# Optimization experiments

Measured on AMD Instinct MI355X. Metric: run time of the kernel, lower is better.

Reference implementation:

```python
import jax, jax.numpy as jnp
import numpy as np

N_NODES = 100000
N_EDGES = 1600000
FEAT, HID, OUT = 256, 128, 64
N_BATCH = 10000
EPS = 1e-5


def gcn_conv(x, src, dst, W, b, n):
    # PyG GCNConv: linear -> add self loops -> sym-normalized scatter-add -> bias
    h = x @ W  # [N, C]
    loop = jnp.arange(n, dtype=src.dtype)
    s = jnp.concatenate([src, loop])
    d = jnp.concatenate([dst, loop])
    deg = jax.ops.segment_sum(jnp.ones_like(d, dtype=h.dtype), d, num_segments=n)
    dinv = jnp.where(deg > 0, jax.lax.rsqrt(deg), 0.0)
    norm = dinv[s] * dinv[d]                    # [E+N]
    msg = h[s] * norm[:, None]                  # gather + scale
    out = jax.ops.segment_sum(msg, d, num_segments=n)  # scatter-add
    return out + b


def batch_norm(x, gamma, beta):
    # training-mode BatchNorm1d: batch statistics, biased variance
    mu = jnp.mean(x, axis=0)
    var = jnp.var(x, axis=0)
    return (x - mu) * jax.lax.rsqrt(var + EPS) * gamma + beta


def setup_inputs() -> dict:
    key = jax.random.key(0)
    ks = jax.random.split(key, 8)
    features = jax.random.normal(ks[0], (N_NODES, FEAT), dtype=jnp.float32)
    edge_index = jax.random.randint(ks[1], (2, N_EDGES), 0, N_NODES, dtype=jnp.int64 if jax.config.jax_enable_x64 else jnp.int32)
    batch_nodes = jax.random.randint(ks[2], (N_BATCH,), 0, N_NODES, dtype=jnp.int32)
    W1 = jax.random.normal(ks[3], (FEAT, HID), dtype=jnp.float32) * (1.0 / np.sqrt(FEAT))
    b1 = jnp.zeros((HID,), jnp.float32)
    gamma1 = jnp.ones((HID,), jnp.float32)
    beta1 = jnp.zeros((HID,), jnp.float32)
    W2 = jax.random.normal(ks[4], (HID, OUT), dtype=jnp.float32) * (1.0 / np.sqrt(HID))
    b2 = jnp.zeros((OUT,), jnp.float32)
    gamma2 = jnp.ones((OUT,), jnp.float32)
    beta2 = jnp.zeros((OUT,), jnp.float32)
    return {"features": features, "edge_index": edge_index, "batch_nodes": batch_nodes,
            "W1": W1, "b1": b1, "gamma1": gamma1, "beta1": beta1,
            "W2": W2, "b2": b2, "gamma2": gamma2, "beta2": beta2}


def reference(features, edge_index, batch_nodes, W1, b1, gamma1, beta1, W2, b2, gamma2, beta2):
    src, dst = edge_index[0], edge_index[1]
    n = features.shape[0]
    x = gcn_conv(features, src, dst, W1, b1, n)
    x = jax.nn.relu(batch_norm(x, gamma1, beta1))
    # dropout treated as identity (deterministic reference)
    x = gcn_conv(x, src, dst, W2, b2, n)
    x = jax.nn.relu(batch_norm(x, gamma2, beta2))
    return jax.nn.log_softmax(x[batch_nodes], axis=1)
```

## Files before the change

### kernel.cpp

```cpp
#include <hip/hip_runtime.h>
#include <stdint.h>

typedef unsigned short bf16_t;

constexpr int kNN   = 100000;
constexpr int kNE   = 1600000;
constexpr int kFEAT = 256;
constexpr int kHID  = 128;
constexpr int kOUT  = 64;
constexpr int kNB   = 10000;
constexpr float kEPS = 1e-5f;

constexpr int kEPB  = 4096;
constexpr int kNBLK = (kNE + kEPB - 1) / kEPB;
constexpr int kNBUK = (kNN + 511) / 512;

typedef __attribute__((ext_vector_type(8))) short short8v;
typedef __attribute__((ext_vector_type(4))) float f32x4;

__device__ __forceinline__ float bf2f(bf16_t u) {
    union { uint32_t i; float f; } v; v.i = ((uint32_t)u) << 16; return v.f;
}
__device__ __forceinline__ bf16_t f2bf(float f) {
    uint32_t u = __float_as_uint(f);
    uint32_t r = (u + 0x7FFFu + ((u >> 16) & 1u)) >> 16;
    return (bf16_t)r;
}
__device__ __forceinline__ float lo16(uint32_t u) {
    union { uint32_t i; float f; } v; v.i = u << 16; return v.f;
}
__device__ __forceinline__ float hi16(uint32_t u) {
    union { uint32_t i; float f; } v; v.i = u & 0xFFFF0000u; return v.f;
}


__global__ void k_hist1(const int* __restrict__ ei, const int* __restrict__ flags,
                        unsigned int* __restrict__ counts) {
    __shared__ unsigned int lh[kNBUK];
    int t = threadIdx.x;
    for (int i = t; i < kNBUK; i += 256) lh[i] = 0u;
    __syncthreads();
    int i64 = flags[1];
    int base = blockIdx.x * kEPB;
    for (int k = 0; k < 16; k++) {
        int e = base + k * 256 + t;
        if (e < kNE) {
            int d = i64 ? ei[2 * (kNE + e)] : ei[kNE + e];
            atomicAdd(&lh[d >> 9], 1u);
        }
    }
    __syncthreads();
    for (int i = t; i < kNBUK; i += 256) counts[(size_t)i * kNBLK + blockIdx.x] = lh[i];
}

__global__ void k_scanA(const unsigned int* __restrict__ counts, unsigned int* __restrict__ base,
                        float* __restrict__ stats) {
    __shared__ unsigned int ss[256];
    int t = threadIdx.x;
    for (int i = t; i < 384; i += 256) stats[i] = 0.f;
    unsigned int tot = 0u;
    if (t < kNBUK) {
        const unsigned int* row = counts + (size_t)t * kNBLK;
        for (int j = 0; j < kNBLK; j++) tot += row[j];
    }
    ss[t] = tot;
    __syncthreads();
    for (int o = 1; o < 256; o <<= 1) {
        unsigned int x = (t >= o) ? ss[t - o] : 0u;
        __syncthreads();
        ss[t] += x;
        __syncthreads();
    }
    if (t < kNBUK) base[t] = ss[t] - tot;
    if (t == 0) base[kNBUK] = ss[255];
}

__global__ void k_scanB(const unsigned int* __restrict__ counts, const unsigned int* __restrict__ base,
                        unsigned int* __restrict__ off) {
    __shared__ unsigned int ss[64];
    int b = blockIdx.x, t = threadIdx.x;
    unsigned int run = base[b];
    for (int c0 = 0; c0 < kNBLK; c0 += 64) {
        int idx = c0 + t;
        unsigned int v = (idx < kNBLK) ? counts[(size_t)b * kNBLK + idx] : 0u;
        ss[t] = v;
        __syncthreads();
        for (int o = 1; o < 64; o <<= 1) {
            unsigned int x = (t >= o) ? ss[t - o] : 0u;
            __syncthreads();
            ss[t] += x;
            __syncthreads();
        }
        if (idx < kNBLK) off[(size_t)b * kNBLK + idx] = run + ss[t] - v;
        unsigned int ctot = ss[63];
        __syncthreads();
        run += ctot;
    }
}

__global__ void k_scatter1(const int* __restrict__ ei, const int* __restrict__ flags,
                           const unsigned int* __restrict__ off, unsigned int* __restrict__ pairs) {
    __shared__ unsigned int lcur[kNBUK];
    int t = threadIdx.x;
    for (int i = t; i < kNBUK; i += 256) lcur[i] = off[(size_t)i * kNBLK + blockIdx.x];
    __syncthreads();
    int i64 = flags[1];
    int base = blockIdx.x * kEPB;
    for (int k = 0; k < 16; k++) {
        int e = base + k * 256 + t;
        if (e < kNE) {
            int s, d;
            if (i64) { s = ei[2 * e]; d = ei[2 * (kNE + e)]; }
            else     { s = ei[e];     d = ei[kNE + e]; }
            unsigned int p = atomicAdd(&lcur[d >> 9], 1u);
            pairs[p] = (unsigned int)s | ((unsigned int)(d & 511) << 17);
        }
    }
}

__global__ void __launch_bounds__(1024) k_scatter2(const unsigned int* __restrict__ pairs,
                        const unsigned int* __restrict__ base, unsigned int* __restrict__ deg,
                        float* __restrict__ dinv, unsigned int* __restrict__ cursor,
                        int* __restrict__ sorted) {
    __shared__ unsigned int hist[512], sc[512], lcur[512];
    int b = blockIdx.x, t = threadIdx.x;
    unsigned int gb = base[b];
    int cnt = (int)(base[b + 1] - gb);
    if (t < 512) hist[t] = 0u;
    __syncthreads();
    for (int i = t; i < cnt; i += 1024) atomicAdd(&hist[pairs[gb + i] >> 17], 1u);
    __syncthreads();
    if (t < 512) sc[t] = hist[t];
    __syncthreads();
    for (int o = 1; o < 512; o <<= 1) {
        unsigned int x = 0u;
        if (t < 512 && t >= o) x = sc[t - o];
        __syncthreads();
        if (t < 512) sc[t] += x;
        __syncthreads();
    }
    if (t < 512) {
        lcur[t] = gb + sc[t] - hist[t];
        int node = b * 512 + t;
        if (node < kNN) {
            unsigned int dg = hist[t] + 1u;
            deg[node] = dg;
            dinv[node] = rsqrtf((float)dg);
            cursor[node] = gb + sc[t];
        }
    }
    __syncthreads();
    for (int i = t; i < cnt; i += 1024) {
        unsigned int pk = pairs[gb + i];
        unsigned int slot = atomicAdd(&lcur[pk >> 17], 1u);
        sorted[slot] = (int)(pk & 0x1FFFFu);
    }
}

__global__ void k_prepw(const void* __restrict__ W1, const void* __restrict__ W2,
                        const uint32_t* __restrict__ feat, const uint32_t* __restrict__ ei,
                        int* __restrict__ flags, bf16_t* __restrict__ Wz1,
                        bf16_t* __restrict__ Wz2) {
    int t = threadIdx.x;
    int good = 0;
    for (int j = t & 63; j < 256; j += 64) {
        uint32_t ex = (feat[j] >> 7) & 0xFFu;
        if (ex >= 100u && ex <= 132u) good++;
    }
    for (int o = 32; o; o >>= 1) good += __shfl_xor(good, o);
    int isbf = (good > 128) ? 1 : 0;
    if (blockIdx.x == 0) {
        int zeros = 0;
        for (int j = t & 63; j < 128; j += 64) zeros += (ei[2 * j + 1] == 0u) ? 1 : 0;
        for (int o = 32; o; o >>= 1) zeros += __shfl_xor(zeros, o);
        if (t == 0) {
            flags[0] = isbf;
            flags[1] = (zeros > 64) ? 1 : 0;
        }
    }
    int gid = blockIdx.x * 256 + t;
    if (gid < 4096) {
        int idx = gid;
        int l = idx & 63, j = (idx >> 6) & 7, tt = idx >> 9;
        int col = j * 16 + (l & 15);
        int kb = tt * 32 + (l >> 4) * 8;
        bf16_t o[8];
        if (isbf) {
            const bf16_t* Wb = (const bf16_t*)W1;
            #pragma unroll
            for (int i = 0; i < 8; i++) o[i] = Wb[(size_t)(kb + i) * kHID + col];
        } else {
            const float* Wf = (const float*)W1;
            #pragma unroll
            for (int i = 0; i < 8; i++) o[i] = f2bf(Wf[(size_t)(kb + i) * kHID + col]);
        }
        uint4 w;
        w.x = (uint32_t)o[0] | ((uint32_t)o[1] << 16);
        w.y = (uint32_t)o[2] | ((uint32_t)o[3] << 16);
        w.z = (uint32_t)o[4] | ((uint32_t)o[5] << 16);
        w.w = (uint32_t)o[6] | ((uint32_t)o[7] << 16);
        *(uint4*)(Wz1 + (size_t)idx * 8) = w;
    } else if (gid < 4096 + 1024) {
        int idx = gid - 4096;
        int l = idx & 63, j = (idx >> 6) & 3, tt = idx >> 8;
        int col = j * 16 + (l & 15);
        int kb = tt * 32 + (l >> 4) * 8;
        bf16_t o[8];
        if (isbf) {
            const bf16_t* Wb = (const bf16_t*)W2;
            #pragma unroll
            for (int i = 0; i < 8; i++) o[i] = Wb[(size_t)(kb + i) * kOUT + col];
        } else {
            const float* Wf = (const float*)W2;
            #pragma unroll
            for (int i = 0; i < 8; i++) o[i] = f2bf(Wf[(size_t)(kb + i) * kOUT + col]);
        }
        uint4 w;
        w.x = (uint32_t)o[0] | ((uint32_t)o[1] << 16);
        w.y = (uint32_t)o[2] | ((uint32_t)o[3] << 16);
        w.z = (uint32_t)o[4] | ((uint32_t)o[5] << 16);
        w.w = (uint32_t)o[6] | ((uint32_t)o[7] << 16);
        *(uint4*)(Wz2 + (size_t)idx * 8) = w;
    }
}

__global__ void k_gemm1(const void* __restrict__ A, const bf16_t* __restrict__ Wz,
                        const float* __restrict__ dinv, bf16_t* __restrict__ H,
                        const int* __restrict__ flags) {
    int isbf = flags[0];
    int wv = threadIdx.x >> 6;
    int l  = threadIdx.x & 63;
    int kgrp = l >> 4;
    int rbase = blockIdx.x * 128 + wv * 32;
    int arow0 = rbase + (l & 15);
    int arow1 = arow0 + 16;
    const bf16_t* Ab = (const bf16_t*)A;
    const float*  Af = (const float*)A;
    const short8v* Wv = (const short8v*)Wz;

    f32x4 acc[2][8];
    #pragma unroll
    for (int m = 0; m < 2; m++)
        #pragma unroll
        for (int j = 0; j < 8; j++)
            acc[m][j] = (f32x4){0.f, 0.f, 0.f, 0.f};

    #pragma unroll
    for (int t = 0; t < 8; t++) {
        int kbase = t * 32 + kgrp * 8;
        short8v a0, a1;
        #pragma unroll
        for (int i = 0; i < 8; i++) { a0[i] = 0; a1[i] = 0; }
        if (arow0 < kNN) {
            if (isbf) {
                a0 = *(const short8v*)(Ab + (size_t)arow0 * kFEAT + kbase);
            } else {
                const float* p = Af + (size_t)arow0 * kFEAT + kbase;
                #pragma unroll
                for (int i = 0; i < 8; i++) a0[i] = (short)f2bf(p[i]);
            }
        }
        if (arow1 < kNN) {
            if (isbf) {
                a1 = *(const short8v*)(Ab + (size_t)arow1 * kFEAT + kbase);
            } else {
                const float* p = Af + (size_t)arow1 * kFEAT + kbase;
                #pragma unroll
                for (int i = 0; i < 8; i++) a1[i] = (short)f2bf(p[i]);
            }
        }
        #pragma unroll
        for (int j = 0; j < 8; j++) {
            short8v b = Wv[(t * 8 + j) * 64 + l];
            acc[0][j] = __builtin_amdgcn_mfma_f32_16x16x32_bf16(a0, b, acc[0][j], 0, 0, 0);
            acc[1][j] = __builtin_amdgcn_mfma_f32_16x16x32_bf16(a1, b, acc[1][j], 0, 0, 0);
        }
    }

    #pragma unroll
    for (int m = 0; m < 2; m++) {
        #pragma unroll
        for (int r = 0; r < 4; r++) {
            int orow = rbase + m * 16 + kgrp * 4 + r;
            if (orow < kNN) {
                float dn = dinv[orow];
                bf16_t* hp = H + (size_t)orow * kHID + (l & 15);
                #pragma unroll
                for (int j = 0; j < 8; j++) hp[j * 16] = f2bf(acc[m][j][r] * dn);
            }
        }
    }
}

__global__ void k_agg1(const bf16_t* __restrict__ H, const int* __restrict__ sorted,
                       const unsigned int* __restrict__ cursor, const unsigned int* __restrict__ deg,
                       const float* __restrict__ dinv, const void* __restrict__ bias,
                       const int* __restrict__ flags, float* __restrict__ Out) {
    int t = threadIdx.x;
    int wv = t >> 6;
    int lane = t & 63;
    int c0 = lane * 2;
    int n = __builtin_amdgcn_readfirstlane(blockIdx.x * 4 + wv);
    float b0, b1v;
    if (flags[0]) { b0 = bf2f(((const bf16_t*)bias)[c0]); b1v = bf2f(((const bf16_t*)bias)[c0 + 1]); }
    else          { b0 = ((const float*)bias)[c0];        b1v = ((const float*)bias)[c0 + 1]; }
    const uint32_t* Hrow = (const uint32_t*)H;
    float dn = dinv[n];
    uint32_t hu = Hrow[(size_t)n * 64 + lane];
    float acc0 = lo16(hu), acc1 = hi16(hu);
    unsigned int e1 = cursor[n];
    int cnt = (int)(deg[n] - 1u);
    unsigned int e = e1 - (unsigned int)cnt;
    for (; cnt >= 8; cnt -= 8, e += 8) {
        int s0 = sorted[e],     s1 = sorted[e + 1], s2 = sorted[e + 2], s3 = sorted[e + 3];
        int s4 = sorted[e + 4], s5 = sorted[e + 5], s6 = sorted[e + 6], s7 = sorted[e + 7];
        uint32_t u0 = Hrow[(size_t)s0 * 64 + lane];
        uint32_t u1 = Hrow[(size_t)s1 * 64 + lane];
        uint32_t u2 = Hrow[(size_t)s2 * 64 + lane];
        uint32_t u3 = Hrow[(size_t)s3 * 64 + lane];
        uint32_t u4 = Hrow[(size_t)s4 * 64 + lane];
        uint32_t u5 = Hrow[(size_t)s5 * 64 + lane];
        uint32_t u6 = Hrow[(size_t)s6 * 64 + lane];
        uint32_t u7 = Hrow[(size_t)s7 * 64 + lane];
        acc0 += lo16(u0) + lo16(u1) + lo16(u2) + lo16(u3)
              + lo16(u4) + lo16(u5) + lo16(u6) + lo16(u7);
        acc1 += hi16(u0) + hi16(u1) + hi16(u2) + hi16(u3)
              + hi16(u4) + hi16(u5) + hi16(u6) + hi16(u7);
    }
    for (; cnt > 0; cnt--, e++) {
        uint32_t u = Hrow[(size_t)sorted[e] * 64 + lane];
        acc0 += lo16(u);
        acc1 += hi16(u);
    }
    float2 o; o.x = acc0 * dn + b0; o.y = acc1 * dn + b1v;
    *(float2*)(Out + (size_t)n * kHID + c0) = o;
}

__global__ void k_stat1(const float* __restrict__ A1, float* __restrict__ stats) {
    int c = threadIdx.x & 127;
    int r0 = threadIdx.x >> 7;
    int chunk = (kNN + gridDim.x - 1) / gridDim.x;
    int nbeg = blockIdx.x * chunk;
    int nend = nbeg + chunk; if (nend > kNN) nend = kNN;
    float s0 = 0.f, s1 = 0.f;
    for (int n = nbeg + r0; n < nend; n += 2) {
        float v = A1[(size_t)n * kHID + c];
        s0 += v; s1 += v * v;
    }
    atomicAdd(&stats[c], s0);
    atomicAdd(&stats[kHID + c], s1);
}

__global__ void k_bnprep(const float* __restrict__ stats, const void* __restrict__ gamma,
                         const void* __restrict__ beta, const int* __restrict__ flags,
                         float* __restrict__ bnp) {
    int c = threadIdx.x;
    float mu = stats[c] * (1.f / kNN);
    float var = stats[128 + c] * (1.f / kNN) - mu * mu;
    float rs = rsqrtf(var + kEPS);
    float g, b;
    if (flags[0]) { g = bf2f(((const bf16_t*)gamma)[c]); b = bf2f(((const bf16_t*)beta)[c]); }
    else          { g = ((const float*)gamma)[c];        b = ((const float*)beta)[c]; }
    float sc = rs * g;
    bnp[c] = sc;
    bnp[128 + c] = b - mu * sc;
}

__global__ void k_gemm2(const float* A, const bf16_t* __restrict__ Wz,
                        const float* __restrict__ dinv, const float* __restrict__ bnp,
                        bf16_t* H ) {
    int wv = threadIdx.x >> 6;
    int l  = threadIdx.x & 63;
    int kgrp = l >> 4;
    int rbase = blockIdx.x * 128 + wv * 32;
    int arow0 = rbase + (l & 15);
    int arow1 = arow0 + 16;
    const short8v* Wv = (const short8v*)Wz;

    f32x4 acc[2][4];
    #pragma unroll
    for (int m = 0; m < 2; m++)
        #pragma unroll
        for (int j = 0; j < 4; j++)
            acc[m][j] = (f32x4){0.f, 0.f, 0.f, 0.f};

    #pragma unroll
    for (int t = 0; t < 4; t++) {
        int kbase = t * 32 + kgrp * 8;
        float4 sa = *(const float4*)(bnp + kbase);
        float4 sb = *(const float4*)(bnp + kbase + 4);
        float4 ha = *(const float4*)(bnp + 128 + kbase);
        float4 hb = *(const float4*)(bnp + 128 + kbase + 4);
        short8v a0, a1;
        #pragma unroll
        for (int i = 0; i < 8; i++) { a0[i] = 0; a1[i] = 0; }
        if (arow0 < kNN) {
            float4 f0 = *(const float4*)(A + (size_t)arow0 * kHID + kbase);
            float4 f1 = *(const float4*)(A + (size_t)arow0 * kHID + kbase + 4);
            float v;
            v = f0.x * sa.x + ha.x; a0[0] = (short)f2bf(v > 0.f ? v : 0.f);
            v = f0.y * sa.y + ha.y; a0[1] = (short)f2bf(v > 0.f ? v : 0.f);
            v = f0.z * sa.z + ha.z; a0[2] = (short)f2bf(v > 0.f ? v : 0.f);
            v = f0.w * sa.w + ha.w; a0[3] = (short)f2bf(v > 0.f ? v : 0.f);
            v = f1.x * sb.x + hb.x; a0[4] = (short)f2bf(v > 0.f ? v : 0.f);
            v = f1.y * sb.y + hb.y; a0[5] = (short)f2bf(v > 0.f ? v : 0.f);
            v = f1.z * sb.z + hb.z; a0[6] = (short)f2bf(v > 0.f ? v : 0.f);
            v = f1.w * sb.w + hb.w; a0[7] = (short)f2bf(v > 0.f ? v : 0.f);
        }
        if (arow1 < kNN) {
            float4 f0 = *(const float4*)(A + (size_t)arow1 * kHID + kbase);
            float4 f1 = *(const float4*)(A + (size_t)arow1 * kHID + kbase + 4);
            float v;
            v = f0.x * sa.x + ha.x; a1[0] = (short)f2bf(v > 0.f ? v : 0.f);
            v = f0.y * sa.y + ha.y; a1[1] = (short)f2bf(v > 0.f ? v : 0.f);
            v = f0.z * sa.z + ha.z; a1[2] = (short)f2bf(v > 0.f ? v : 0.f);
            v = f0.w * sa.w + ha.w; a1[3] = (short)f2bf(v > 0.f ? v : 0.f);
            v = f1.x * sb.x + hb.x; a1[4] = (short)f2bf(v > 0.f ? v : 0.f);
            v = f1.y * sb.y + hb.y; a1[5] = (short)f2bf(v > 0.f ? v : 0.f);
            v = f1.z * sb.z + hb.z; a1[6] = (short)f2bf(v > 0.f ? v : 0.f);
            v = f1.w * sb.w + hb.w; a1[7] = (short)f2bf(v > 0.f ? v : 0.f);
        }
        #pragma unroll
        for (int j = 0; j < 4; j++) {
            short8v b = Wv[(t * 4 + j) * 64 + l];
            acc[0][j] = __builtin_amdgcn_mfma_f32_16x16x32_bf16(a0, b, acc[0][j], 0, 0, 0);
            acc[1][j] = __builtin_amdgcn_mfma_f32_16x16x32_bf16(a1, b, acc[1][j], 0, 0, 0);
        }
    }

    #pragma unroll
    for (int m = 0; m < 2; m++) {
        #pragma unroll
        for (int r = 0; r < 4; r++) {
            int orow = rbase + m * 16 + kgrp * 4 + r;
            if (orow < kNN) {
                float dn = dinv[orow];
                bf16_t* hp = H + (size_t)orow * 256 + (l & 15);
                #pragma unroll
                for (int j = 0; j < 4; j++) hp[j * 16] = f2bf(acc[m][j][r] * dn);
            }
        }
    }
}

__global__ void k_agg2(const bf16_t* __restrict__ H, const int* __restrict__ sorted,
                       const unsigned int* __restrict__ cursor, const unsigned int* __restrict__ deg,
                       const float* __restrict__ dinv, const void* __restrict__ bias,
                       const int* __restrict__ flags, float* __restrict__ Out) {
    int t = threadIdx.x;
    int wv = t >> 6;
    int lane = t & 63;
    int half = lane >> 5;
    int w32 = lane & 31;
    int c0 = w32 * 2;
    int n = __builtin_amdgcn_readfirstlane(blockIdx.x * 4 + wv);
    float b0, b1v;
    if (flags[0]) { b0 = bf2f(((const bf16_t*)bias)[c0]); b1v = bf2f(((const bf16_t*)bias)[c0 + 1]); }
    else          { b0 = ((const float*)bias)[c0];        b1v = ((const float*)bias)[c0 + 1]; }
    const uint32_t* Hrow = (const uint32_t*)H;
    float dn = dinv[n];
    uint32_t hu = Hrow[(size_t)n * 128 + w32];
    float acc0 = half ? 0.f : lo16(hu);
    float acc1 = half ? 0.f : hi16(hu);
    unsigned int e1 = cursor[n];
    int cnt = (int)(deg[n] - 1u);
    unsigned int e = e1 - (unsigned int)cnt;
    for (; cnt >= 16; cnt -= 16, e += 16) {
        int s0 = sorted[e],      s1 = sorted[e + 1],  s2 = sorted[e + 2],  s3 = sorted[e + 3];
        int s4 = sorted[e + 4],  s5 = sorted[e + 5],  s6 = sorted[e + 6],  s7 = sorted[e + 7];
        int s8 = sorted[e + 8],  s9 = sorted[e + 9],  sa = sorted[e + 10], sb = sorted[e + 11];
        int sc = sorted[e + 12], sd = sorted[e + 13], se = sorted[e + 14], sf = sorted[e + 15];
        int i0 = half ? s1 : s0;
        int i1 = half ? s3 : s2;
        int i2 = half ? s5 : s4;
        int i3 = half ? s7 : s6;
        int i4 = half ? s9 : s8;
        int i5 = half ? sb : sa;
        int i6 = half ? sd : sc;
        int i7 = half ? sf : se;
        uint32_t u0 = Hrow[(size_t)i0 * 128 + w32];
        uint32_t u1 = Hrow[(size_t)i1 * 128 + w32];
        uint32_t u2 = Hrow[(size_t)i2 * 128 + w32];
        uint32_t u3 = Hrow[(size_t)i3 * 128 + w32];
        uint32_t u4 = Hrow[(size_t)i4 * 128 + w32];
        uint32_t u5 = Hrow[(size_t)i5 * 128 + w32];
        uint32_t u6 = Hrow[(size_t)i6 * 128 + w32];
        uint32_t u7 = Hrow[(size_t)i7 * 128 + w32];
        acc0 += lo16(u0) + lo16(u1) + lo16(u2) + lo16(u3)
              + lo16(u4) + lo16(u5) + lo16(u6) + lo16(u7);
        acc1 += hi16(u0) + hi16(u1) + hi16(u2) + hi16(u3)
              + hi16(u4) + hi16(u5) + hi16(u6) + hi16(u7);
    }
    for (; cnt >= 2; cnt -= 2, e += 2) {
        int sA = sorted[e], sB = sorted[e + 1];
        int si = half ? sB : sA;
        uint32_t u = Hrow[(size_t)si * 128 + w32];
        acc0 += lo16(u);
        acc1 += hi16(u);
    }
    if (cnt) {
        uint32_t u = Hrow[(size_t)sorted[e] * 128 + w32];
        if (!half) { acc0 += lo16(u); acc1 += hi16(u); }
    }
    acc0 += __shfl_xor(acc0, 32);
    acc1 += __shfl_xor(acc1, 32);
    if (!half) {
        float2 o; o.x = acc0 * dn + b0; o.y = acc1 * dn + b1v;
        *(float2*)(Out + (size_t)n * kOUT + c0) = o;
    }
}

__global__ void k_stat2(const float* __restrict__ A2, float* __restrict__ stats) {
    int c = threadIdx.x & 63;
    int r0 = threadIdx.x >> 6;
    int chunk = (kNN + gridDim.x - 1) / gridDim.x;
    int nbeg = blockIdx.x * chunk;
    int nend = nbeg + chunk; if (nend > kNN) nend = kNN;
    float s0 = 0.f, s1 = 0.f;
    for (int n = nbeg + r0; n < nend; n += 4) {
        float v = A2[(size_t)n * kOUT + c];
        s0 += v; s1 += v * v;
    }
    atomicAdd(&stats[256 + c], s0);
    atomicAdd(&stats[320 + c], s1);
}

__global__ void k_out(const float* __restrict__ A2, const float* __restrict__ stats,
                      const int* __restrict__ batch, const void* __restrict__ gamma,
                      const void* __restrict__ beta, const int* __restrict__ flags,
                      bf16_t* __restrict__ out) {
    int wid = threadIdx.x >> 6;
    int lane = threadIdx.x & 63;
    int i = blockIdx.x * 4 + wid;
    if (i >= kNB) return;
    int n = batch[i];
    int c = lane;
    float mu = stats[256 + c] * (1.f / kNN);
    float var = stats[320 + c] * (1.f / kNN) - mu * mu;
    float g, b;
    if (flags[0]) { g = bf2f(((const bf16_t*)gamma)[c]); b = bf2f(((const bf16_t*)beta)[c]); }
    else          { g = ((const float*)gamma)[c];        b = ((const float*)beta)[c]; }
    float v = (A2[(size_t)n * kOUT + c] - mu) * rsqrtf(var + kEPS) * g + b;
    v = v > 0.f ? v : 0.f;
    float m = v;
    for (int o = 32; o; o >>= 1) m = fmaxf(m, __shfl_xor(m, o));
    float ex = expf(v - m);
    float s = ex;
    for (int o = 32; o; o >>= 1) s += __shfl_xor(s, o);
    float r = v - m - logf(s);
    if (flags[0]) out[(size_t)i * kOUT + c] = f2bf(r);
    else ((float*)out)[(size_t)i * kOUT + c] = r;
}

static inline size_t align_up(size_t x, size_t a) { return (x + a - 1) & ~(a - 1); }

extern "C" void kernel_launch(void* const* d_in, const int* in_sizes, int n_in,
                              void* d_out, int out_size, void* d_ws, size_t ws_size,
                              hipStream_t stream) {
    (void)in_sizes; (void)n_in; (void)out_size; (void)ws_size;
    const void* feat = d_in[0];
    const int* ei    = (const int*)d_in[1];
    const int* batch = (const int*)d_in[2];
    const void* W1   = d_in[3];
    const void* b1   = d_in[4];
    const void* g1   = d_in[5];
    const void* be1  = d_in[6];
    const void* W2   = d_in[7];
    const void* b2   = d_in[8];
    const void* g2   = d_in[9];
    const void* be2  = d_in[10];

    char* ws = (char*)d_ws;
    size_t o = 0;
    int*          flags  = (int*)(ws + o);          o = align_up(o + 32, 256);
    unsigned int* deg    = (unsigned int*)(ws + o); o = align_up(o + (size_t)kNN * 4, 256);
    float*        dinv   = (float*)(ws + o);        o = align_up(o + (size_t)kNN * 4, 256);
    unsigned int* cursor = (unsigned int*)(ws + o); o = align_up(o + (size_t)kNN * 4, 256);
    float*        stats  = (float*)(ws + o);        o = align_up(o + 384 * 4, 256);
    float*        bnp    = (float*)(ws + o);        o = align_up(o + 256 * 4, 256);
    int*          sorted = (int*)(ws + o);          o = align_up(o + (size_t)kNE * 4, 256);
    bf16_t*       h1     = (bf16_t*)(ws + o);       o = align_up(o + (size_t)kNN * kHID * 2, 256);
    float*        a1     = (float*)(ws + o);        o = align_up(o + (size_t)kNN * kHID * 4, 256);
    bf16_t*       wz1    = (bf16_t*)(ws + o);       o = align_up(o + (size_t)8 * 8 * 64 * 8 * 2, 256);
    bf16_t*       wz2    = (bf16_t*)(ws + o);       o = align_up(o + (size_t)4 * 4 * 64 * 8 * 2, 256);

    unsigned int* pairs  = (unsigned int*)h1;
    unsigned int* counts = (unsigned int*)a1;
    unsigned int* offm   = (unsigned int*)((char*)a1 + 512 * 1024);
    unsigned int* gbase  = (unsigned int*)((char*)a1 + 1024 * 1024);

    bf16_t*       h2 = (bf16_t*)a1;
    float*        a2 = (float*)h1;

    bf16_t* outp = (bf16_t*)d_out;

    k_prepw   <<<20, 256, 0, stream>>>(W1, W2, (const uint32_t*)feat, (const uint32_t*)ei,
                                       flags, wz1, wz2);
    k_hist1   <<<kNBLK, 256, 0, stream>>>(ei, flags, counts);
    k_scanA   <<<1, 256, 0, stream>>>(counts, gbase, stats);
    k_scanB   <<<kNBUK, 64, 0, stream>>>(counts, gbase, offm);
    k_scatter1<<<kNBLK, 256, 0, stream>>>(ei, flags, offm, pairs);
    k_scatter2<<<kNBUK, 1024, 0, stream>>>(pairs, gbase, deg, dinv, cursor, sorted);

    k_gemm1 <<<(kNN + 127) / 128, 256, 0, stream>>>(feat, wz1, dinv, h1, flags);
    k_agg1  <<<kNN / 4, 256, 0, stream>>>(h1, sorted, cursor, deg, dinv, b1, flags, a1);
    k_stat1 <<<256, 256, 0, stream>>>(a1, stats);
    k_bnprep<<<1, 128, 0, stream>>>(stats, g1, be1, flags, bnp);

    k_gemm2<<<(kNN + 127) / 128, 256, 0, stream>>>(a1, wz2, dinv, bnp, h2);
    k_agg2 <<<kNN / 4, 256, 0, stream>>>(h2, sorted, cursor, deg, dinv, b2, flags, a2);
    k_stat2<<<256, 256, 0, stream>>>(a2, stats);

    k_out<<<(kNB + 3) / 4, 256, 0, stream>>>(a2, stats, batch, g2, be2, flags, outp);
}
```

Baseline: 493.1 us.

## Column-slice H1 layout for aggregation and replace scanA row sums with atomic totals

GEMM1 now writes H1 in eight column-group planes of 16 features each, and agg1 runs eight blocks per node group. Each lane group gathers 32-byte slices from neighbours in parallel across edges, then reduces with shuffles, so each plane (~3.2MB) can stay cache-resident during the random gathers. The histogram kernel also accumulates per-bucket totals atomically, which removes the serial per-bucket row sums in scanA. The cost is eight times more blocks, extra shuffle reductions and redundant index loads per column group.

Result: slower. 703.6 us (+42.7%).

```diff
diff --git a/kernel.cpp b/kernel.cpp
--- a/kernel.cpp
+++ b/kernel.cpp
@@ -17,6 +17,7 @@
 
 typedef __attribute__((ext_vector_type(8))) short short8v;
 typedef __attribute__((ext_vector_type(4))) float f32x4;
+typedef __attribute__((ext_vector_type(2))) float f32x2;
 
 __device__ __forceinline__ float bf2f(bf16_t u) {
     union { uint32_t i; float f; } v; v.i = ((uint32_t)u) << 16; return v.f;
@@ -35,7 +36,7 @@
 
 
 __global__ void k_hist1(const int* __restrict__ ei, const int* __restrict__ flags,
-                        unsigned int* __restrict__ counts) {
+                        unsigned int* __restrict__ counts, unsigned int* __restrict__ btot) {
     __shared__ unsigned int lh[kNBUK];
     int t = threadIdx.x;
     for (int i = t; i < kNBUK; i += 256) lh[i] = 0u;
@@ -50,19 +51,18 @@
         }
     }
     __syncthreads();
-    for (int i = t; i < kNBUK; i += 256) counts[(size_t)i * kNBLK + blockIdx.x] = lh[i];
-}
-
-__global__ void k_scanA(const unsigned int* __restrict__ counts, unsigned int* __restrict__ base,
+    for (int i = t; i < kNBUK; i += 256) {
+        counts[(size_t)i * kNBLK + blockIdx.x] = lh[i];
+        if (lh[i]) atomicAdd(&btot[i], lh[i]);
+    }
+}
+
+__global__ void k_scanA(const unsigned int* __restrict__ btot, unsigned int* __restrict__ base,
                         float* __restrict__ stats) {
     __shared__ unsigned int ss[256];
     int t = threadIdx.x;
     for (int i = t; i < 384; i += 256) stats[i] = 0.f;
-    unsigned int tot = 0u;
-    if (t < kNBUK) {
-        const unsigned int* row = counts + (size_t)t * kNBLK;
-        for (int j = 0; j < kNBLK; j++) tot += row[j];
-    }
+    unsigned int tot = (t < kNBUK) ? btot[t] : 0u;
     ss[t] = tot;
     __syncthreads();
     for (int o = 1; o < 256; o <<= 1) {
@@ -160,7 +160,7 @@
 __global__ void k_prepw(const void* __restrict__ W1, const void* __restrict__ W2,
                         const uint32_t* __restrict__ feat, const uint32_t* __restrict__ ei,
                         int* __restrict__ flags, bf16_t* __restrict__ Wz1,
-                        bf16_t* __restrict__ Wz2) {
+                        bf16_t* __restrict__ Wz2, unsigned int* __restrict__ btot) {
     int t = threadIdx.x;
     int good = 0;
     for (int j = t & 63; j < 256; j += 64) {
@@ -221,6 +221,8 @@
         w.z = (uint32_t)o[4] | ((uint32_t)o[5] << 16);
         w.w = (uint32_t)o[6] | ((uint32_t)o[7] << 16);
         *(uint4*)(Wz2 + (size_t)idx * 8) = w;
+    } else if (gid < 4096 + 1024 + kNBUK) {
+        btot[gid - 5120] = 0u;
     }
 }
 
@@ -284,9 +286,9 @@
             int orow = rbase + m * 16 + kgrp * 4 + r;
             if (orow < kNN) {
                 float dn = dinv[orow];
-                bf16_t* hp = H + (size_t)orow * kHID + (l & 15);
                 #pragma unroll
-                for (int j = 0; j < 8; j++) hp[j * 16] = f2bf(acc[m][j][r] * dn);
+                for (int j = 0; j < 8; j++)
+                    H[((size_t)j * kNN + orow) * 16 + (l & 15)] = f2bf(acc[m][j][r] * dn);
             }
         }
     }
@@ -299,41 +301,52 @@
     int t = threadIdx.x;
     int wv = t >> 6;
     int lane = t & 63;
-    int c0 = lane * 2;
-    int n = __builtin_amdgcn_readfirstlane(blockIdx.x * 4 + wv);
-    float b0, b1v;
-    if (flags[0]) { b0 = bf2f(((const bf16_t*)bias)[c0]); b1v = bf2f(((const bf16_t*)bias)[c0 + 1]); }
-    else          { b0 = ((const float*)bias)[c0];        b1v = ((const float*)bias)[c0 + 1]; }
-    const uint32_t* Hrow = (const uint32_t*)H;
-    float dn = dinv[n];
-    uint32_t hu = Hrow[(size_t)n * 64 + lane];
-    float acc0 = lo16(hu), acc1 = hi16(hu);
+    int q = lane >> 3;
+    int cp = lane & 7;
+    int g = __builtin_amdgcn_readfirstlane(blockIdx.x & 7);
+    int n = __builtin_amdgcn_readfirstlane((blockIdx.x >> 3) * 4 + wv);
+    const uint32_t* Hg = (const uint32_t*)H + (size_t)g * kNN * 8;
+
+    float acc0 = 0.f, acc1 = 0.f;
     unsigned int e1 = cursor[n];
     int cnt = (int)(deg[n] - 1u);
     unsigned int e = e1 - (unsigned int)cnt;
+    for (; cnt >= 16; cnt -= 16, e += 16) {
+        int ia = __builtin_nontemporal_load(sorted + e + q);
+        int ib = __builtin_nontemporal_load(sorted + e + 8 + q);
+        uint32_t ua = Hg[(size_t)ia * 8 + cp];
+        uint32_t ub = Hg[(size_t)ib * 8 + cp];
+        acc0 += lo16(ua) + lo16(ub);
+        acc1 += hi16(ua) + hi16(ub);
+    }
     for (; cnt >= 8; cnt -= 8, e += 8) {
-        int s0 = sorted[e],     s1 = sorted[e + 1], s2 = sorted[e + 2], s3 = sorted[e + 3];
-        int s4 = sorted[e + 4], s5 = sorted[e + 5], s6 = sorted[e + 6], s7 = sorted[e + 7];
-        uint32_t u0 = Hrow[(size_t)s0 * 64 + lane];
-        uint32_t u1 = Hrow[(size_t)s1 * 64 + lane];
-        uint32_t u2 = Hrow[(size_t)s2 * 64 + lane];
-        uint32_t u3 = Hrow[(size_t)s3 * 64 + lane];
-        uint32_t u4 = Hrow[(size_t)s4 * 64 + lane];
-        uint32_t u5 = Hrow[(size_t)s5 * 64 + lane];
-        uint32_t u6 = Hrow[(size_t)s6 * 64 + lane];
-        uint32_t u7 = Hrow[(size_t)s7 * 64 + lane];
-        acc0 += lo16(u0) + lo16(u1) + lo16(u2) + lo16(u3)
-              + lo16(u4) + lo16(u5) + lo16(u6) + lo16(u7);
-        acc1 += hi16(u0) + hi16(u1) + hi16(u2) + hi16(u3)
-              + hi16(u4) + hi16(u5) + hi16(u6) + hi16(u7);
-    }
-    for (; cnt > 0; cnt--, e++) {
-        uint32_t u = Hrow[(size_t)sorted[e] * 64 + lane];
-        acc0 += lo16(u);
-        acc1 += hi16(u);
-    }
-    float2 o; o.x = acc0 * dn + b0; o.y = acc1 * dn + b1v;
-    *(float2*)(Out + (size_t)n * kHID + c0) = o;
+        int ia = __builtin_nontemporal_load(sorted + e + q);
+        uint32_t ua = Hg[(size_t)ia * 8 + cp];
+        acc0 += lo16(ua);
+        acc1 += hi16(ua);
+    }
+    if (cnt > 0) {
+        int ia = __builtin_nontemporal_load(sorted + e + (q < cnt ? q : 0));
+        uint32_t ua = Hg[(size_t)ia * 8 + cp];
+        if (q < cnt) { acc0 += lo16(ua); acc1 += hi16(ua); }
+    }
+    acc0 += __shfl_xor(acc0, 8);  acc1 += __shfl_xor(acc1, 8);
+    acc0 += __shfl_xor(acc0, 16); acc1 += __shfl_xor(acc1, 16);
+    acc0 += __shfl_xor(acc0, 32); acc1 += __shfl_xor(acc1, 32);
+    if (lane < 8) {
+        uint32_t hu = Hg[(size_t)n * 8 + cp];
+        acc0 += lo16(hu);
+        acc1 += hi16(hu);
+        int c0 = g * 16 + cp * 2;
+        float b0, b1v;
+        if (flags[0]) { b0 = bf2f(((const bf16_t*)bias)[c0]); b1v = bf2f(((const bf16_t*)bias)[c0 + 1]); }
+        else          { b0 = ((const float*)bias)[c0];        b1v = ((const float*)bias)[c0 + 1]; }
+        float dn = dinv[n];
+        f32x2 o;
+        o.x = acc0 * dn + b0;
+        o.y = acc1 * dn + b1v;
+        __builtin_nontemporal_store(o, (f32x2*)(Out + (size_t)n * kHID + c0));
+    }
 }
 
 __global__ void k_stat1(const float* __restrict__ A1, float* __restrict__ stats) {
@@ -578,6 +591,7 @@
     unsigned int* cursor = (unsigned int*)(ws + o); o = align_up(o + (size_t)kNN * 4, 256);
     float*        stats  = (float*)(ws + o);        o = align_up(o + 384 * 4, 256);
     float*        bnp    = (float*)(ws + o);        o = align_up(o + 256 * 4, 256);
+    unsigned int* btot   = (unsigned int*)(ws + o); o = align_up(o + 256 * 4, 256);
     int*          sorted = (int*)(ws + o);          o = align_up(o + (size_t)kNE * 4, 256);
     bf16_t*       h1     = (bf16_t*)(ws + o);       o = align_up(o + (size_t)kNN * kHID * 2, 256);
     float*        a1     = (float*)(ws + o);        o = align_up(o + (size_t)kNN * kHID * 4, 256);
@@ -594,16 +608,16 @@
 
     bf16_t* outp = (bf16_t*)d_out;
 
-    k_prepw   <<<20, 256, 0, stream>>>(W1, W2, (const uint32_t*)feat, (const uint32_t*)ei,
-                                       flags, wz1, wz2);
-    k_hist1   <<<kNBLK, 256, 0, stream>>>(ei, flags, counts);
-    k_scanA   <<<1, 256, 0, stream>>>(counts, gbase, stats);
+    k_prepw   <<<21, 256, 0, stream>>>(W1, W2, (const uint32_t*)feat, (const uint32_t*)ei,
+                                       flags, wz1, wz2, btot);
+    k_hist1   <<<kNBLK, 256, 0, stream>>>(ei, flags, counts, btot);
+    k_scanA   <<<1, 256, 0, stream>>>(btot, gbase, stats);
     k_scanB   <<<kNBUK, 64, 0, stream>>>(counts, gbase, offm);
     k_scatter1<<<kNBLK, 256, 0, stream>>>(ei, flags, offm, pairs);
     k_scatter2<<<kNBUK, 1024, 0, stream>>>(pairs, gbase, deg, dinv, cursor, sorted);
 
     k_gemm1 <<<(kNN + 127) / 128, 256, 0, stream>>>(feat, wz1, dinv, h1, flags);
-    k_agg1  <<<kNN / 4, 256, 0, stream>>>(h1, sorted, cursor, deg, dinv, b1, flags, a1);
+    k_agg1  <<<(kNN / 4) * 8, 256, 0, stream>>>(h1, sorted, cursor, deg, dinv, b1, flags, a1);
     k_stat1 <<<256, 256, 0, stream>>>(a1, stats);
     k_bnprep<<<1, 128, 0, stream>>>(stats, g1, be1, flags, bnp);
 
```
